# Optimization experiments

Hardware: AMD Instinct MI355X
Metric: run time of the kernel (lower is better)

The kernel has to match this reference:

```python
import jax, jax.numpy as jnp
import numpy as np
from jax import lax

B, T = 64, 2048
D_LSTM, D_ENC, D_ATT, N_F, K = 1024, 512, 128, 32, 31
PAD = (K - 1) // 2  # 15, 'same' padding as Tacotron2 LocationLayer


def setup_inputs() -> dict:
    key = jax.random.key(0)
    ks = jax.random.split(key, 11)
    def w(k, shape, fan_in):
        return jax.random.normal(k, shape, dtype=jnp.float32) / np.sqrt(fan_in)
    return {
        "query": jax.random.normal(ks[0], (B, 1, D_LSTM), dtype=jnp.float32),
        "memory": jax.random.normal(ks[1], (B, T, D_ENC), dtype=jnp.float32),
        "attention_weights_cat": jax.random.uniform(ks[2], (B, 2, T), dtype=jnp.float32),
        "Wq": w(ks[3], (D_ATT, D_LSTM), D_LSTM),
        "bq": jnp.zeros((D_ATT,), jnp.float32),
        "Wm": w(ks[4], (D_ATT, D_ENC), D_ENC),
        "bm": jnp.zeros((D_ATT,), jnp.float32),
        "Wconv": w(ks[5], (N_F, 2, K), 2 * K),  # Conv1d weight [out, in, k], bias=False
        "Wloc": w(ks[6], (D_ATT, N_F), N_F),     # location dense, bias=False
        "Wv": w(ks[7], (1, D_ATT), D_ATT),
        "bv": jnp.zeros((1,), jnp.float32),
    }


def reference(query, memory, attention_weights_cat, Wq, bq, Wm, bm, Wconv, Wloc, Wv, bv):
    # query_layer: [B,1,D_LSTM] -> [B,1,D_ATT]
    q = query @ Wq.T + bq
    # memory_layer: [B,T,D_ENC] -> [B,T,D_ATT]
    k = memory @ Wm.T + bm
    # location_layer: Conv1d same-pad over time, then dense to D_ATT
    conv = lax.conv_general_dilated(
        attention_weights_cat, Wconv, window_strides=(1,),
        padding=[(PAD, PAD)], dimension_numbers=("NCH", "OIH", "NCH"))  # [B,N_F,T]
    loc = jnp.einsum("bft,af->bta", conv, Wloc)  # [B,T,D_ATT]
    # energies: v^T tanh(q + k + loc) -> [B,T]
    energies = (jnp.tanh(q + k + loc) @ Wv.T + bv).squeeze(-1)
    attention_weights = jax.nn.softmax(energies, axis=1)  # [B,T]
    attention_context = jnp.einsum("bt,btd->bd", attention_weights, memory)  # [B,D_ENC]
    return attention_context, attention_weights
```

## Files before the change

### kernel.cpp

```cpp
#include <hip/hip_runtime.h>
#include <math.h>

#define B_ 64
#define T_ 2048
#define DL 1024
#define DE 512
#define DA 128
#define NF 32
#define KW 31
#define PADW 15
#define TT 128

typedef short bf16x8 __attribute__((ext_vector_type(8)));
typedef float f32x4 __attribute__((ext_vector_type(4)));

__device__ __forceinline__ int frag_off(int row, int kin) {
    return (((row >> 4) * 64 + (kin >> 3) * 16 + (row & 15)) << 3) + (kin & 7);
}

__device__ __forceinline__ void split2_trunc(float x0, float x1, unsigned &h01, unsigned &l01) {
    unsigned u0 = __float_as_uint(x0), u1 = __float_as_uint(x1);
    h01 = __builtin_amdgcn_perm(u1, u0, 0x07060302u);
    float l0 = x0 - __uint_as_float(u0 & 0xFFFF0000u);
    float l1 = x1 - __uint_as_float(u1 & 0xFFFF0000u);
    l01 = __builtin_amdgcn_perm(__float_as_uint(l1), __float_as_uint(l0), 0x07060302u);
}

__device__ __forceinline__ void split1_trunc(float x, unsigned short &h, unsigned short &l) {
    unsigned u = __float_as_uint(x);
    h = (unsigned short)(u >> 16);
    float lf = x - __uint_as_float(u & 0xFFFF0000u);
    l = (unsigned short)(__float_as_uint(lf) >> 16);
}

__device__ __forceinline__ float fast_tanh(float x) {
    x = fminf(fmaxf(x, -15.f), 15.f);
    float e2 = __expf(2.f * x);
    return (e2 - 1.f) * __builtin_amdgcn_rcpf(e2 + 1.f);
}

__global__ __launch_bounds__(256) void prep_kernel(const float* __restrict__ Wm,
                                                   unsigned short* __restrict__ Bsw) {
    int i = blockIdx.x * 256 + threadIdx.x;
    int a = i >> 9, k = i & 511;
    float x = Wm[i];
    unsigned u = __float_as_uint(x);
    unsigned short h = (unsigned short)((u + 0x7FFFu + ((u >> 16) & 1u)) >> 16);
    float lf = x - __uint_as_float((unsigned)h << 16);
    unsigned ul = __float_as_uint(lf);
    unsigned short l = (unsigned short)((ul + 0x7FFFu + ((ul >> 16) & 1u)) >> 16);
    int c = k >> 5, kin = k & 31;
    size_t base = (size_t)c * 8192 + frag_off(a, kin);
    Bsw[base] = h;
    Bsw[base + 4096] = l;
}

__global__ __launch_bounds__(128) void q_kernel(const float* __restrict__ query,
                                                const float* __restrict__ Wq,
                                                const float* __restrict__ bq,
                                                float* __restrict__ qbuf) {
    int b = blockIdx.x;
    int a = threadIdx.x;
    __shared__ __align__(16) float qs[DL];
    for (int i = threadIdx.x; i < DL; i += 128) qs[i] = query[(size_t)b * DL + i];
    __syncthreads();
    const float* wrow = Wq + (size_t)a * DL;
    float acc = 0.f;
#pragma unroll 8
    for (int i = 0; i < DL; i += 4) {
        float4 w = *(const float4*)(wrow + i);
        float4 q4 = *(const float4*)(qs + i);
        acc += w.x * q4.x + w.y * q4.y + w.z * q4.z + w.w * q4.w;
    }
    qbuf[(size_t)b * DA + a] = acc + bq[a];
}

__global__ __launch_bounds__(256, 3) void energy_kernel(
    const float* __restrict__ mem,
    const float* __restrict__ attw,
    const unsigned short* __restrict__ Bsw,
    const float* __restrict__ bm,
    const float* __restrict__ Wconv,
    const float* __restrict__ Wloc,
    const float* __restrict__ Wv,
    const float* __restrict__ bv,
    const float* __restrict__ qbuf,
    float* __restrict__ e_out)
{
    __shared__ __align__(16) unsigned short Abuf[8192];
    __shared__ __align__(16) unsigned short Bbuf[2][8192];
    __shared__ float qb_s[DA], wv_s[DA];
    __shared__ float e_part[2][TT];

    const int tid = threadIdx.x;
    const int b = blockIdx.y;
    const int t0 = blockIdx.x * TT;
    const int lane = tid & 63;
    const int wave = tid >> 6;
    const int wm = wave & 1, wn = wave >> 1;
    const int m = lane & 15;

    float* attw_s  = (float*)Bbuf[1];
    float* wconv_s = (float*)Bbuf[1] + 320;

    if (tid < DA) {
        qb_s[tid] = qbuf[(size_t)b * DA + tid] + bm[tid];
        wv_s[tid] = Wv[tid];
    }

    for (int i = tid; i < 2 * (TT + KW - 1); i += 256) {
        int c = i / 158, j = i % 158;
        int t = t0 - PADW + j;
        attw_s[c * 160 + j] = (t >= 0 && t < T_) ? attw[((size_t)b * 2 + c) * T_ + t] : 0.f;
    }
    for (int i = tid; i < NF * 2 * KW; i += 256) {
        int f = i / 62, r = i % 62;
        wconv_s[f * 64 + r] = Wconv[i];
    }
    for (int i = tid; i < DA * NF; i += 256) {
        int a = i >> 5, f = i & 31;
        unsigned short h, l;
        split1_trunc(Wloc[a * NF + f], h, l);
        int off = frag_off(a, f);
        Bbuf[0][off] = h;
        Bbuf[0][off + 4096] = l;
    }
    __syncthreads();

    for (int i = tid; i < TT * NF; i += 256) {
        int t = i >> 5, f = i & 31;
        const float* w0 = wconv_s + f * 64;
        const float* a0 = attw_s + t;
        const float* a1 = attw_s + 160 + t;
        float s = 0.f;
#pragma unroll
        for (int k = 0; k < KW; ++k) s += w0[k] * a0[k] + w0[31 + k] * a1[k];
        unsigned short h, l;
        split1_trunc(s, h, l);
        int off = frag_off(t, f);
        Abuf[off] = h;
        Abuf[off + 4096] = l;
    }
    __syncthreads();

    f32x4 acc[4][4];
#pragma unroll
    for (int mi = 0; mi < 4; ++mi)
#pragma unroll
        for (int ni = 0; ni < 4; ++ni) {
            f32x4 z = {0.f, 0.f, 0.f, 0.f};
            acc[mi][ni] = z;
        }

    auto mfma_step = [&](const unsigned short* Bb) {
        bf16x8 ah[4], al[4];
#pragma unroll
        for (int mi = 0; mi < 4; ++mi) {
            const unsigned short* p = Abuf + (((wm * 4 + mi) * 64 + lane) << 3);
            ah[mi] = *(const bf16x8*)p;
            al[mi] = *(const bf16x8*)(p + 4096);
        }
#pragma unroll
        for (int ni = 0; ni < 4; ++ni) {
            const unsigned short* p = Bb + (((wn * 4 + ni) * 64 + lane) << 3);
            bf16x8 bh = *(const bf16x8*)p;
            bf16x8 bl = *(const bf16x8*)(p + 4096);
#pragma unroll
            for (int mi = 0; mi < 4; ++mi) {
                acc[mi][ni] = __builtin_amdgcn_mfma_f32_16x16x32_bf16(ah[mi], bh, acc[mi][ni], 0, 0, 0);
                acc[mi][ni] = __builtin_amdgcn_mfma_f32_16x16x32_bf16(ah[mi], bl, acc[mi][ni], 0, 0, 0);
                acc[mi][ni] = __builtin_amdgcn_mfma_f32_16x16x32_bf16(al[mi], bh, acc[mi][ni], 0, 0, 0);
            }
        }
    };

    auto issue_B = [&](int c, unsigned short* dst) {
        const unsigned char* g = (const unsigned char*)Bsw + (size_t)c * 16384 + wave * 4096 + lane * 16;
        unsigned char* l = (unsigned char*)dst + wave * 4096;
#pragma unroll
        for (int it = 0; it < 4; ++it)
            __builtin_amdgcn_global_load_lds(
                (const __attribute__((address_space(1))) unsigned*)(g + it * 1024),
                (__attribute__((address_space(3))) unsigned*)(l + it * 1024), 16, 0, 0);
    };

    const size_t mem_base = ((size_t)b * T_ + t0) * DE;
    const int tA = tid >> 3;
    const int c4 = (tid & 7) * 4;

    float4 ap[4];
    auto load_A = [&](int c) {
        const float* p = mem + mem_base + (size_t)tA * DE + c * 32 + c4;
#pragma unroll
        for (int r = 0; r < 4; ++r) ap[r] = *(const float4*)(p + (size_t)r * 32 * DE);
    };
    auto store_A = [&]() {
        int off0 = frag_off(tA, c4);
#pragma unroll
        for (int r = 0; r < 4; ++r) {
            unsigned h01, l01, h23, l23;
            split2_trunc(ap[r].x, ap[r].y, h01, l01);
            split2_trunc(ap[r].z, ap[r].w, h23, l23);
            int off = off0 + r * 1024;
            uint2 hv = {h01, h23}, lv = {l01, l23};
            *(uint2*)(Abuf + off) = hv;
            *(uint2*)(Abuf + off + 4096) = lv;
        }
    };

    mfma_step(Bbuf[0]);
    load_A(0);
    __syncthreads();
    issue_B(0, Bbuf[0]);
    store_A();
    __syncthreads();

    for (int c = 0; c < 16; ++c) {
        if (c < 15) {
            load_A(c + 1);
            issue_B(c + 1, Bbuf[(c + 1) & 1]);
        }
        mfma_step(Bbuf[c & 1]);
        __syncthreads();
        if (c < 15) store_A();
        __syncthreads();
    }

    float wvr[4], qbr[4];
#pragma unroll
    for (int ni = 0; ni < 4; ++ni) {
        int a = wn * 64 + ni * 16 + m;
        wvr[ni] = wv_s[a];
        qbr[ni] = qb_s[a];
    }
    float bvv = bv[0];
#pragma unroll
    for (int mi = 0; mi < 4; ++mi) {
#pragma unroll
        for (int reg = 0; reg < 4; ++reg) {
            float s = 0.f;
#pragma unroll
            for (int ni = 0; ni < 4; ++ni)
                s += wvr[ni] * fast_tanh(acc[mi][ni][reg] + qbr[ni]);
            s += __shfl_xor(s, 1, 64);
            s += __shfl_xor(s, 2, 64);
            s += __shfl_xor(s, 4, 64);
            s += __shfl_xor(s, 8, 64);
            if (m == 0)
                e_part[wn][wm * 64 + mi * 16 + (lane >> 4) * 4 + reg] = s;
        }
    }
    __syncthreads();
    if (tid < TT)
        e_out[(size_t)b * T_ + t0 + tid] = e_part[0][tid] + e_part[1][tid] + bvv;
}

__global__ __launch_bounds__(256) void softmax_kernel(const float* __restrict__ e,
                                                      float* __restrict__ wout) {
    int b = blockIdx.x;
    int tid = threadIdx.x;
    __shared__ float red[4];
    float v[8];
    float m = -1e30f;
#pragma unroll
    for (int r = 0; r < 8; ++r) {
        v[r] = e[(size_t)b * T_ + r * 256 + tid];
        m = fmaxf(m, v[r]);
    }
#pragma unroll
    for (int off = 1; off < 64; off <<= 1) m = fmaxf(m, __shfl_xor(m, off, 64));
    if ((tid & 63) == 0) red[tid >> 6] = m;
    __syncthreads();
    m = fmaxf(fmaxf(red[0], red[1]), fmaxf(red[2], red[3]));
    __syncthreads();
    float s = 0.f;
#pragma unroll
    for (int r = 0; r < 8; ++r) {
        v[r] = expf(v[r] - m);
        s += v[r];
    }
#pragma unroll
    for (int off = 1; off < 64; off <<= 1) s += __shfl_xor(s, off, 64);
    if ((tid & 63) == 0) red[tid >> 6] = s;
    __syncthreads();
    s = red[0] + red[1] + red[2] + red[3];
    float inv = 1.0f / s;
#pragma unroll
    for (int r = 0; r < 8; ++r) wout[(size_t)b * T_ + r * 256 + tid] = v[r] * inv;
}

__global__ __launch_bounds__(256) void ctx_partial_kernel(const float* __restrict__ mem,
                                                          const float* __restrict__ w,
                                                          float* __restrict__ partial) {
    int b = blockIdx.y, tc = blockIdx.x;
    int tid = threadIdx.x;
    __shared__ float ws_s[128];
    __shared__ float red[512];
    if (tid < 128) ws_s[tid] = w[(size_t)b * T_ + tc * 128 + tid];
    __syncthreads();
    int d = (tid & 127) * 4;
    int th = tid >> 7;
    const float* mp = mem + ((size_t)b * T_ + tc * 128 + th * 64) * DE + d;
    float a0 = 0.f, a1 = 0.f, a2 = 0.f, a3 = 0.f;
#pragma unroll 8
    for (int t = 0; t < 64; ++t) {
        float4 v = *(const float4*)(mp + (size_t)t * DE);
        float wv = ws_s[th * 64 + t];
        a0 += wv * v.x; a1 += wv * v.y; a2 += wv * v.z; a3 += wv * v.w;
    }
    if (th == 1) {
        float* r = red + (tid & 127) * 4;
        r[0] = a0; r[1] = a1; r[2] = a2; r[3] = a3;
    }
    __syncthreads();
    if (th == 0) {
        const float* r = red + tid * 4;
        float* pp = partial + ((size_t)b * 16 + tc) * DE + d;
        pp[0] = a0 + r[0]; pp[1] = a1 + r[1]; pp[2] = a2 + r[2]; pp[3] = a3 + r[3];
    }
}

__global__ __launch_bounds__(512) void ctx_reduce_kernel(const float* __restrict__ partial,
                                                         float* __restrict__ ctx) {
    int b = blockIdx.x;
    int d = threadIdx.x;
    float s = 0.f;
#pragma unroll
    for (int j = 0; j < 16; ++j) s += partial[((size_t)b * 16 + j) * DE + d];
    ctx[(size_t)b * DE + d] = s;
}

extern "C" void kernel_launch(void* const* d_in, const int* in_sizes, int n_in,
                              void* d_out, int out_size, void* d_ws, size_t ws_size,
                              hipStream_t stream) {
    const float* query  = (const float*)d_in[0];
    const float* memory = (const float*)d_in[1];
    const float* attw   = (const float*)d_in[2];
    const float* Wq     = (const float*)d_in[3];
    const float* bq     = (const float*)d_in[4];
    const float* Wm     = (const float*)d_in[5];
    const float* bm     = (const float*)d_in[6];
    const float* Wconv  = (const float*)d_in[7];
    const float* Wloc   = (const float*)d_in[8];
    const float* Wv     = (const float*)d_in[9];
    const float* bv     = (const float*)d_in[10];

    float* out = (float*)d_out;
    float* ctx_out = out;
    float* w_out = out + B_ * DE;

    float* ws = (float*)d_ws;
    float* qbuf = ws;
    float* ebuf = qbuf + B_ * DA;
    float* partial = ebuf + (size_t)B_ * T_;
    unsigned short* Bsw = (unsigned short*)(partial + (size_t)B_ * 16 * DE);

    prep_kernel<<<dim3(DA * DE / 256), dim3(256), 0, stream>>>(Wm, Bsw);
    q_kernel<<<dim3(B_), dim3(128), 0, stream>>>(query, Wq, bq, qbuf);
    energy_kernel<<<dim3(T_ / TT, B_), dim3(256), 0, stream>>>(
        memory, attw, Bsw, bm, Wconv, Wloc, Wv, bv, qbuf, ebuf);
    softmax_kernel<<<dim3(B_), dim3(256), 0, stream>>>(ebuf, w_out);
    ctx_partial_kernel<<<dim3(16, B_), dim3(256), 0, stream>>>(memory, w_out, partial);
    ctx_reduce_kernel<<<dim3(B_), dim3(512), 0, stream>>>(partial, ctx_out);
}
```

Before: 567.9 us.

## Stream fp32 memory tiles directly to LDS and split to bf16 at fragment load

```diff
diff --git a/kernel.cpp b/kernel.cpp
--- a/kernel.cpp
+++ b/kernel.cpp
@@ -14,9 +14,7 @@
 typedef short bf16x8 __attribute__((ext_vector_type(8)));
 typedef float f32x4 __attribute__((ext_vector_type(4)));
 
-__device__ __forceinline__ int frag_off(int row, int kin) {
-    return (((row >> 4) * 64 + (kin >> 3) * 16 + (row & 15)) << 3) + (kin & 7);
-}
+union BF8 { bf16x8 v; unsigned u[4]; };
 
 __device__ __forceinline__ void split2_trunc(float x0, float x1, unsigned &h01, unsigned &l01) {
     unsigned u0 = __float_as_uint(x0), u1 = __float_as_uint(x1);
@@ -37,6 +35,15 @@
     x = fminf(fmaxf(x, -15.f), 15.f);
     float e2 = __expf(2.f * x);
     return (e2 - 1.f) * __builtin_amdgcn_rcpf(e2 + 1.f);
+}
+
+__device__ __forceinline__ int frag_off(int row, int kin) {
+    return (((row >> 4) * 64 + (kin >> 3) * 16 + (row & 15)) << 3) + (kin & 7);
+}
+
+__device__ __forceinline__ int a_fidx(int r, int k) {
+    int unit = ((r >> 4) << 7) + (((k >> 2) & 1) << 6) + ((k >> 3) << 4) + (r & 15);
+    return (unit << 2) + (k & 3);
 }
 
 __global__ __launch_bounds__(256) void prep_kernel(const float* __restrict__ Wm,
@@ -75,7 +82,7 @@
     qbuf[(size_t)b * DA + a] = acc + bq[a];
 }
 
-__global__ __launch_bounds__(256, 3) void energy_kernel(
+__global__ __launch_bounds__(256, 2) void energy_kernel(
     const float* __restrict__ mem,
     const float* __restrict__ attw,
     const unsigned short* __restrict__ Bsw,
@@ -87,7 +94,7 @@
     const float* __restrict__ qbuf,
     float* __restrict__ e_out)
 {
-    __shared__ __align__(16) unsigned short Abuf[8192];
+    __shared__ __align__(16) float Abuf[2][4096];
     __shared__ __align__(16) unsigned short Bbuf[2][8192];
     __shared__ float qb_s[DA], wv_s[DA];
     __shared__ float e_part[2][TT];
@@ -98,16 +105,16 @@
     const int lane = tid & 63;
     const int wave = tid >> 6;
     const int wm = wave & 1, wn = wave >> 1;
-    const int m = lane & 15;
-
-    float* attw_s  = (float*)Bbuf[1];
-    float* wconv_s = (float*)Bbuf[1] + 320;
+    const int m15 = lane & 15;
+    const int kg = lane >> 4;
+
+    float* attw_s  = Abuf[1];
+    float* wconv_s = Abuf[1] + 320;
 
     if (tid < DA) {
         qb_s[tid] = qbuf[(size_t)b * DA + tid] + bm[tid];
         wv_s[tid] = Wv[tid];
     }
-
     for (int i = tid; i < 2 * (TT + KW - 1); i += 256) {
         int c = i / 158, j = i % 158;
         int t = t0 - PADW + j;
@@ -122,8 +129,8 @@
         unsigned short h, l;
         split1_trunc(Wloc[a * NF + f], h, l);
         int off = frag_off(a, f);
-        Bbuf[0][off] = h;
-        Bbuf[0][off + 4096] = l;
+        Bbuf[1][off] = h;
+        Bbuf[1][off + 4096] = l;
     }
     __syncthreads();
 
@@ -135,11 +142,7 @@
         float s = 0.f;
 #pragma unroll
         for (int k = 0; k < KW; ++k) s += w0[k] * a0[k] + w0[31 + k] * a1[k];
-        unsigned short h, l;
-        split1_trunc(s, h, l);
-        int off = frag_off(t, f);
-        Abuf[off] = h;
-        Abuf[off + 4096] = l;
+        Abuf[0][a_fidx(t, f)] = s;
     }
     __syncthreads();
 
@@ -152,84 +155,83 @@
             acc[mi][ni] = z;
         }
 
-    auto mfma_step = [&](const unsigned short* Bb) {
-        bf16x8 ah[4], al[4];
+    const size_t mem_base = ((size_t)b * T_ + t0) * DE;
+    const float* aptr[4];
+#pragma unroll
+    for (int it = 0; it < 4; ++it) {
+        int id = wave * 4 + it;
+        int r = (id >> 1) * 16 + m15;
+        int col = kg * 8 + (id & 1) * 4;
+        aptr[it] = mem + mem_base + (size_t)r * DE + col;
+    }
+    const unsigned short* bptr = Bsw + wave * 2048 + lane * 8;
+
+    auto issue_A = [&](float* dst) {
+#pragma unroll
+        for (int it = 0; it < 4; ++it) {
+            __builtin_amdgcn_global_load_lds(
+                (const __attribute__((address_space(1))) unsigned*)aptr[it],
+                (__attribute__((address_space(3))) unsigned*)((char*)dst + (wave * 4 + it) * 1024),
+                16, 0, 0);
+            aptr[it] += 32;
+        }
+    };
+    auto issue_B = [&](unsigned short* dst) {
+#pragma unroll
+        for (int it = 0; it < 4; ++it) {
+            __builtin_amdgcn_global_load_lds(
+                (const __attribute__((address_space(1))) unsigned*)bptr,
+                (__attribute__((address_space(3))) unsigned*)((char*)dst + wave * 4096 + it * 1024),
+                16, 0, 0);
+            bptr += 512;
+        }
+        bptr += 6144;
+    };
+
+    auto mfma_step = [&](const float* Ab, const unsigned short* Bb) {
+        BF8 ah[4], al[4];
 #pragma unroll
         for (int mi = 0; mi < 4; ++mi) {
-            const unsigned short* p = Abuf + (((wm * 4 + mi) * 64 + lane) << 3);
-            ah[mi] = *(const bf16x8*)p;
-            al[mi] = *(const bf16x8*)(p + 4096);
+            const float* p = Ab + (wm * 4 + mi) * 512 + lane * 4;
+            f32x4 a0 = *(const f32x4*)p;
+            f32x4 a1 = *(const f32x4*)(p + 256);
+            split2_trunc(a0.x, a0.y, ah[mi].u[0], al[mi].u[0]);
+            split2_trunc(a0.z, a0.w, ah[mi].u[1], al[mi].u[1]);
+            split2_trunc(a1.x, a1.y, ah[mi].u[2], al[mi].u[2]);
+            split2_trunc(a1.z, a1.w, ah[mi].u[3], al[mi].u[3]);
         }
 #pragma unroll
         for (int ni = 0; ni < 4; ++ni) {
-            const unsigned short* p = Bb + (((wn * 4 + ni) * 64 + lane) << 3);
-            bf16x8 bh = *(const bf16x8*)p;
-            bf16x8 bl = *(const bf16x8*)(p + 4096);
+            const unsigned short* q = Bb + ((wn * 4 + ni) * 64 + lane) * 8;
+            bf16x8 bh = *(const bf16x8*)q;
+            bf16x8 bl = *(const bf16x8*)(q + 4096);
 #pragma unroll
             for (int mi = 0; mi < 4; ++mi) {
-                acc[mi][ni] = __builtin_amdgcn_mfma_f32_16x16x32_bf16(ah[mi], bh, acc[mi][ni], 0, 0, 0);
-                acc[mi][ni] = __builtin_amdgcn_mfma_f32_16x16x32_bf16(ah[mi], bl, acc[mi][ni], 0, 0, 0);
-                acc[mi][ni] = __builtin_amdgcn_mfma_f32_16x16x32_bf16(al[mi], bh, acc[mi][ni], 0, 0, 0);
+                acc[mi][ni] = __builtin_amdgcn_mfma_f32_16x16x32_bf16(ah[mi].v, bh, acc[mi][ni], 0, 0, 0);
+                acc[mi][ni] = __builtin_amdgcn_mfma_f32_16x16x32_bf16(ah[mi].v, bl, acc[mi][ni], 0, 0, 0);
+                acc[mi][ni] = __builtin_amdgcn_mfma_f32_16x16x32_bf16(al[mi].v, bh, acc[mi][ni], 0, 0, 0);
             }
         }
     };
 
-    auto issue_B = [&](int c, unsigned short* dst) {
-        const unsigned char* g = (const unsigned char*)Bsw + (size_t)c * 16384 + wave * 4096 + lane * 16;
-        unsigned char* l = (unsigned char*)dst + wave * 4096;
-#pragma unroll
-        for (int it = 0; it < 4; ++it)
-            __builtin_amdgcn_global_load_lds(
-                (const __attribute__((address_space(1))) unsigned*)(g + it * 1024),
-                (__attribute__((address_space(3))) unsigned*)(l + it * 1024), 16, 0, 0);
-    };
-
-    const size_t mem_base = ((size_t)b * T_ + t0) * DE;
-    const int tA = tid >> 3;
-    const int c4 = (tid & 7) * 4;
-
-    float4 ap[4];
-    auto load_A = [&](int c) {
-        const float* p = mem + mem_base + (size_t)tA * DE + c * 32 + c4;
-#pragma unroll
-        for (int r = 0; r < 4; ++r) ap[r] = *(const float4*)(p + (size_t)r * 32 * DE);
-    };
-    auto store_A = [&]() {
-        int off0 = frag_off(tA, c4);
-#pragma unroll
-        for (int r = 0; r < 4; ++r) {
-            unsigned h01, l01, h23, l23;
-            split2_trunc(ap[r].x, ap[r].y, h01, l01);
-            split2_trunc(ap[r].z, ap[r].w, h23, l23);
-            int off = off0 + r * 1024;
-            uint2 hv = {h01, h23}, lv = {l01, l23};
-            *(uint2*)(Abuf + off) = hv;
-            *(uint2*)(Abuf + off + 4096) = lv;
-        }
-    };
-
-    mfma_step(Bbuf[0]);
-    load_A(0);
-    __syncthreads();
-    issue_B(0, Bbuf[0]);
-    store_A();
+    issue_A(Abuf[1]);
+    issue_B(Bbuf[0]);
+    mfma_step(Abuf[0], Bbuf[1]);
     __syncthreads();
 
     for (int c = 0; c < 16; ++c) {
         if (c < 15) {
-            load_A(c + 1);
-            issue_B(c + 1, Bbuf[(c + 1) & 1]);
-        }
-        mfma_step(Bbuf[c & 1]);
+            issue_A(Abuf[c & 1]);
+            issue_B(Bbuf[(c + 1) & 1]);
+        }
+        mfma_step(Abuf[(c + 1) & 1], Bbuf[c & 1]);
         __syncthreads();
-        if (c < 15) store_A();
-        __syncthreads();
     }
 
     float wvr[4], qbr[4];
 #pragma unroll
     for (int ni = 0; ni < 4; ++ni) {
-        int a = wn * 64 + ni * 16 + m;
+        int a = wn * 64 + ni * 16 + m15;
         wvr[ni] = wv_s[a];
         qbr[ni] = qb_s[a];
     }
@@ -246,8 +248,8 @@
             s += __shfl_xor(s, 2, 64);
             s += __shfl_xor(s, 4, 64);
             s += __shfl_xor(s, 8, 64);
-            if (m == 0)
-                e_part[wn][wm * 64 + mi * 16 + (lane >> 4) * 4 + reg] = s;
+            if (m15 == 0)
+                e_part[wn][wm * 64 + mi * 16 + kg * 4 + reg] = s;
         }
     }
     __syncthreads();
@@ -294,18 +296,18 @@
                                                           float* __restrict__ partial) {
     int b = blockIdx.y, tc = blockIdx.x;
     int tid = threadIdx.x;
-    __shared__ float ws_s[128];
+    __shared__ float ws_s[64];
     __shared__ float red[512];
-    if (tid < 128) ws_s[tid] = w[(size_t)b * T_ + tc * 128 + tid];
+    if (tid < 64) ws_s[tid] = w[(size_t)b * T_ + tc * 64 + tid];
     __syncthreads();
     int d = (tid & 127) * 4;
     int th = tid >> 7;
-    const float* mp = mem + ((size_t)b * T_ + tc * 128 + th * 64) * DE + d;
+    const float* mp = mem + ((size_t)b * T_ + tc * 64 + th * 32) * DE + d;
     float a0 = 0.f, a1 = 0.f, a2 = 0.f, a3 = 0.f;
 #pragma unroll 8
-    for (int t = 0; t < 64; ++t) {
+    for (int t = 0; t < 32; ++t) {
         float4 v = *(const float4*)(mp + (size_t)t * DE);
-        float wv = ws_s[th * 64 + t];
+        float wv = ws_s[th * 32 + t];
         a0 += wv * v.x; a1 += wv * v.y; a2 += wv * v.z; a3 += wv * v.w;
     }
     if (th == 1) {
@@ -315,7 +317,7 @@
     __syncthreads();
     if (th == 0) {
         const float* r = red + tid * 4;
-        float* pp = partial + ((size_t)b * 16 + tc) * DE + d;
+        float* pp = partial + ((size_t)b * 32 + tc) * DE + d;
         pp[0] = a0 + r[0]; pp[1] = a1 + r[1]; pp[2] = a2 + r[2]; pp[3] = a3 + r[3];
     }
 }
@@ -326,7 +328,7 @@
     int d = threadIdx.x;
     float s = 0.f;
 #pragma unroll
-    for (int j = 0; j < 16; ++j) s += partial[((size_t)b * 16 + j) * DE + d];
+    for (int j = 0; j < 32; ++j) s += partial[((size_t)b * 32 + j) * DE + d];
     ctx[(size_t)b * DE + d] = s;
 }
 
@@ -353,13 +355,13 @@
     float* qbuf = ws;
     float* ebuf = qbuf + B_ * DA;
     float* partial = ebuf + (size_t)B_ * T_;
-    unsigned short* Bsw = (unsigned short*)(partial + (size_t)B_ * 16 * DE);
+    unsigned short* Bsw = (unsigned short*)(partial + (size_t)B_ * 32 * DE);
 
     prep_kernel<<<dim3(DA * DE / 256), dim3(256), 0, stream>>>(Wm, Bsw);
     q_kernel<<<dim3(B_), dim3(128), 0, stream>>>(query, Wq, bq, qbuf);
     energy_kernel<<<dim3(T_ / TT, B_), dim3(256), 0, stream>>>(
         memory, attw, Bsw, bm, Wconv, Wloc, Wv, bv, qbuf, ebuf);
     softmax_kernel<<<dim3(B_), dim3(256), 0, stream>>>(ebuf, w_out);
-    ctx_partial_kernel<<<dim3(16, B_), dim3(256), 0, stream>>>(memory, w_out, partial);
+    ctx_partial_kernel<<<dim3(32, B_), dim3(256), 0, stream>>>(memory, w_out, partial);
     ctx_reduce_kernel<<<dim3(B_), dim3(512), 0, stream>>>(partial, ctx_out);
 }
```

Result: slower. 735.0 us (+29.4%).
